# Kernel tuning notes

Measured on AMD Instinct MI355X. Metric: run time of the kernel, lower is better.

The kernel has to match this reference:

```python
import jax, jax.numpy as jnp
import numpy as np

N_EMB = 256
HEAD_SIZE = 64
B, S = 4, 4096


def setup_inputs() -> dict:
    key = jax.random.key(0)
    k1, k2, k3, k4 = jax.random.split(key, 4)
    return {
        "ini_emb": jax.random.normal(k1, (B, S, N_EMB), dtype=jnp.float32),
        "wk": jax.random.normal(k2, (N_EMB, HEAD_SIZE), dtype=jnp.float32) * (N_EMB ** -0.5),
        "wq": jax.random.normal(k3, (N_EMB, HEAD_SIZE), dtype=jnp.float32) * (N_EMB ** -0.5),
        "wv": jax.random.normal(k4, (N_EMB, HEAD_SIZE), dtype=jnp.float32) * (N_EMB ** -0.5),
    }


def reference(ini_emb, wk, wq, wv):
    # projections: [B,S,E] @ [E,H] -> [B,S,H]
    k = ini_emb @ wk
    q = ini_emb @ wq
    v = ini_emb @ wv
    # scores: [B,S,S]; NOTE: source scales by n_emb**-0.5, not head_size**-0.5
    scores = jnp.einsum("bqh,bkh->bqk", q, k) * (N_EMB ** -0.5)
    attn = jax.nn.softmax(scores, axis=-1)
    # output: [B,S,H]
    return jnp.einsum("bqk,bkh->bqh", attn, v)
```

## Files before the change

kernel.cpp:

```cpp
#include <hip/hip_runtime.h>


typedef short short4v __attribute__((ext_vector_type(4)));
typedef short short8v __attribute__((ext_vector_type(8)));
typedef float floatx4 __attribute__((ext_vector_type(4)));
typedef unsigned short u16;
typedef unsigned int u32;

#define SEQ 4096
#define EMB 256
#define HD 64
#define PADA 264

static __device__ __forceinline__ u16 f2bf(float x) {
    union { float f; unsigned u; } v; v.f = x;
    unsigned r = v.u + 0x7FFFu + ((v.u >> 16) & 1u);
    return (u16)(r >> 16);
}

static __device__ __forceinline__ short4v pack_bf4(float a, float b, float c, float d) {
    union { u32 u[2]; short4v s; } x;
    x.u[0] = (u32)f2bf(a) | ((u32)f2bf(b) << 16);
    x.u[1] = (u32)f2bf(c) | ((u32)f2bf(d) << 16);
    return x.s;
}

__global__ __launch_bounds__(256) void prep_w(
    const float* __restrict__ wk, const float* __restrict__ wq, const float* __restrict__ wv,
    u16* __restrict__ wt) {
    const int nt = blockIdx.x;
    const int t = threadIdx.x;
#pragma unroll
    for (int ss = 0; ss < 2; ++ss) {
        int slot = t + ss * 256;
        int kc = slot >> 6, lane = slot & 63;
        int ln15 = lane & 15, lq = lane >> 4;
        int cg = nt * 16 + ln15;
        int mat = cg >> 6, col = cg & 63;
        const float* W = (mat == 0) ? wq : (mat == 1) ? wk : wv;
        const float s = (mat == 0) ? 0.0625f * 1.44269504088896f : 1.0f;
        u32 w4[4];
#pragma unroll
        for (int p = 0; p < 2; ++p) {
#pragma unroll
            for (int d = 0; d < 2; ++d) {
                int e0 = kc * 32 + lq * 8 + p * 4 + d * 2;
                u16 lo = f2bf(W[(e0 + 0) * HD + col] * s);
                u16 hi = f2bf(W[(e0 + 1) * HD + col] * s);
                w4[p * 2 + d] = (u32)lo | ((u32)hi << 16);
            }
        }
        u32* dst = (u32*)wt + ((size_t)(nt * 8 + kc) * 64 + lane) * 4;
        *(uint4*)dst = make_uint4(w4[0], w4[1], w4[2], w4[3]);
    }
}

__global__ __launch_bounds__(256) void proj_mfma(
    const float* __restrict__ emb, const u16* __restrict__ wt,
    u16* __restrict__ qb, u16* __restrict__ kb, u16* __restrict__ vbt) {
    __shared__ u16 a_s[16 * PADA];
    const int t = threadIdx.x;
    const int lane = t & 63;
    const int wave = t >> 6;
    const int ln15 = lane & 15;
    const int lq = lane >> 4;
    const size_t row0 = (size_t)blockIdx.x * 16;

#pragma unroll
    for (int c = 0; c < 4; ++c) {
        int f = t + c * 256;
        int row = f >> 6, e4 = (f & 63) * 4;
        float4 v = *(const float4*)(emb + (row0 + row) * EMB + e4);
        ushort4 o;
        o.x = f2bf(v.x); o.y = f2bf(v.y); o.z = f2bf(v.z); o.w = f2bf(v.w);
        *(ushort4*)&a_s[row * PADA + e4] = o;
    }
    __syncthreads();

    floatx4 acc[3];
#pragma unroll
    for (int j = 0; j < 3; ++j) {
        floatx4 z = { 0.f, 0.f, 0.f, 0.f };
        acc[j] = z;
    }

#pragma unroll
    for (int kc = 0; kc < 8; ++kc) {
        short8v a = *(const short8v*)&a_s[ln15 * PADA + kc * 32 + lq * 8];
#pragma unroll
        for (int j = 0; j < 3; ++j) {
            short8v b = *(const short8v*)(wt + (((size_t)(wave * 3 + j) * 8 + kc) * 64 + lane) * 8);
            acc[j] = __builtin_amdgcn_mfma_f32_16x16x32_bf16(a, b, acc[j], 0, 0, 0);
        }
    }

#pragma unroll
    for (int j = 0; j < 3; ++j) {
        int cg = (wave * 3 + j) * 16 + ln15;
        int mat = cg >> 6, col = cg & 63;
        if (mat < 2) {
            u16* O = (mat == 0) ? qb : kb;
#pragma unroll
            for (int r = 0; r < 4; ++r)
                O[(row0 + lq * 4 + r) * HD + col] = f2bf(acc[j][r]);
        } else {
            ushort4 o4;
            o4.x = f2bf(acc[j][0]); o4.y = f2bf(acc[j][1]);
            o4.z = f2bf(acc[j][2]); o4.w = f2bf(acc[j][3]);
            size_t bidx = row0 >> 12;
            size_t sl = (row0 & 4095) + lq * 4;
            *(ushort4*)&vbt[(bidx * 64 + col) * SEQ + sl] = o4;
        }
    }
}

__global__ __launch_bounds__(256) void attn_kernel(
    const u16* __restrict__ qb, const u16* __restrict__ kb, const u16* __restrict__ vbt,
    float* __restrict__ po, float* __restrict__ pml) {
    __shared__ float ored[64 * 66];
    __shared__ float lred[4 * 64];

    const int t = threadIdx.x;
    const int lane = t & 63;
    const int wave = t >> 6;
    const int ln15 = lane & 15;
    const int lq = lane >> 4;

    const int part = blockIdx.x;
    const int b = part >> 8;
    const int qt = (part >> 2) & 63;
    const int split = part & 3;
    const int q0 = qt * 64;

    const u16* __restrict__ qpb = qb + ((size_t)b * SEQ + q0) * HD;
    const u16* __restrict__ kpb = kb + (size_t)b * SEQ * HD;
    const u16* __restrict__ vpb = vbt + (size_t)b * HD * SEQ;

    short8v qf[4][2];
#pragma unroll
    for (int nt = 0; nt < 4; ++nt)
#pragma unroll
        for (int h = 0; h < 2; ++h)
            qf[nt][h] = *(const short8v*)(qpb + (size_t)(nt * 16 + ln15) * HD + h * 32 + lq * 8);

    floatx4 oacc[4][4];
#pragma unroll
    for (int ht = 0; ht < 4; ++ht)
#pragma unroll
        for (int nt = 0; nt < 4; ++nt) {
            floatx4 z = { 0.f, 0.f, 0.f, 0.f };
            oacc[ht][nt] = z;
        }
    float lacc[4] = { 0.f, 0.f, 0.f, 0.f };

    for (int tt = 0; tt < 16; ++tt) {
        const int kw = (split * 16 + tt) * 64 + wave * 16;

        short8v kf0 = *(const short8v*)(kpb + (size_t)(kw + ln15) * HD + lq * 8);
        short8v kf1 = *(const short8v*)(kpb + (size_t)(kw + ln15) * HD + 32 + lq * 8);
        short4v vf[4];
#pragma unroll
        for (int ht = 0; ht < 4; ++ht)
            vf[ht] = *(const short4v*)(vpb + (size_t)(ht * 16 + ln15) * SEQ + kw + lq * 4);

        floatx4 s[4];
#pragma unroll
        for (int nt = 0; nt < 4; ++nt) {
            floatx4 z = { 0.f, 0.f, 0.f, 0.f };
            s[nt] = __builtin_amdgcn_mfma_f32_16x16x32_bf16(kf0, qf[nt][0], z, 0, 0, 0);
            s[nt] = __builtin_amdgcn_mfma_f32_16x16x32_bf16(kf1, qf[nt][1], s[nt], 0, 0, 0);
        }

        short4v pf[4];
#pragma unroll
        for (int nt = 0; nt < 4; ++nt) {
            float p0 = __builtin_amdgcn_exp2f(s[nt][0]);
            float p1 = __builtin_amdgcn_exp2f(s[nt][1]);
            float p2 = __builtin_amdgcn_exp2f(s[nt][2]);
            float p3 = __builtin_amdgcn_exp2f(s[nt][3]);
            lacc[nt] += (p0 + p1) + (p2 + p3);
            pf[nt] = pack_bf4(p0, p1, p2, p3);
        }

#pragma unroll
        for (int ht = 0; ht < 4; ++ht)
#pragma unroll
            for (int nt = 0; nt < 4; ++nt)
                oacc[ht][nt] = __builtin_amdgcn_mfma_f32_16x16x16bf16_1k(
                    vf[ht], pf[nt], oacc[ht][nt], 0, 0, 0);
    }

#pragma unroll
    for (int nt = 0; nt < 4; ++nt) {
        lacc[nt] += __shfl_xor(lacc[nt], 16);
        lacc[nt] += __shfl_xor(lacc[nt], 32);
    }
    if (lq == 0) {
#pragma unroll
        for (int nt = 0; nt < 4; ++nt)
            lred[wave * 64 + nt * 16 + ln15] = lacc[nt];
    }

    for (int s4 = 0; s4 < 4; ++s4) {
        if (wave == s4) {
#pragma unroll
            for (int ht = 0; ht < 4; ++ht)
#pragma unroll
                for (int nt = 0; nt < 4; ++nt)
#pragma unroll
                    for (int r = 0; r < 4; ++r) {
                        int idx = (ht * 16 + lq * 4 + r) * 66 + nt * 16 + ln15;
                        if (s4 == 0) ored[idx] = oacc[ht][nt][r];
                        else ored[idx] += oacc[ht][nt][r];
                    }
        }
        __syncthreads();
    }

    float* __restrict__ pob = po + (size_t)part * 4096;
#pragma unroll
    for (int i = 0; i < 16; ++i) {
        int f = t + i * 256;
        pob[f] = ored[(f >> 6) * 66 + (f & 63)];
    }
    if (t < 64)
        pml[part * 64 + t] = lred[t] + lred[64 + t] + lred[128 + t] + lred[192 + t];
}

__global__ __launch_bounds__(256) void reduce_kernel(
    const float* __restrict__ po, const float* __restrict__ pml,
    float* __restrict__ out) {
    __shared__ float os[64 * 67];
    __shared__ float ls[64];
    const int t = threadIdx.x;
    const int part0 = blockIdx.x * 4;
    const int bq = blockIdx.x;

#pragma unroll
    for (int i = 0; i < 16; ++i) {
        int f = t + i * 256;
        float a = po[(size_t)(part0 + 0) * 4096 + f] + po[(size_t)(part0 + 1) * 4096 + f]
                + po[(size_t)(part0 + 2) * 4096 + f] + po[(size_t)(part0 + 3) * 4096 + f];
        os[(f >> 6) * 67 + (f & 63)] = a;
    }
    if (t < 64)
        ls[t] = pml[(part0 + 0) * 64 + t] + pml[(part0 + 1) * 64 + t]
              + pml[(part0 + 2) * 64 + t] + pml[(part0 + 3) * 64 + t];
    __syncthreads();

    const size_t orow0 = ((size_t)(bq >> 6) * SEQ + (size_t)(bq & 63) * 64);
#pragma unroll
    for (int i = 0; i < 4; ++i) {
        int f4 = t + i * 256;
        int q = f4 >> 4, h4 = (f4 & 15) * 4;
        float inv = 1.0f / ls[q];
        float4 r;
        r.x = os[(h4 + 0) * 67 + q] * inv;
        r.y = os[(h4 + 1) * 67 + q] * inv;
        r.z = os[(h4 + 2) * 67 + q] * inv;
        r.w = os[(h4 + 3) * 67 + q] * inv;
        *(float4*)&out[(orow0 + q) * HD + h4] = r;
    }
}

extern "C" void kernel_launch(void* const* d_in, const int* in_sizes, int n_in,
                              void* d_out, int out_size, void* d_ws, size_t ws_size,
                              hipStream_t stream) {
    const float* emb = (const float*)d_in[0];
    const float* wk  = (const float*)d_in[1];
    const float* wq  = (const float*)d_in[2];
    const float* wv  = (const float*)d_in[3];

    u16* qb  = (u16*)d_ws;
    u16* kb  = (u16*)((char*)d_ws + (size_t)2 * 1024 * 1024);
    u16* vbt = (u16*)((char*)d_ws + (size_t)4 * 1024 * 1024);
    u16* wt  = (u16*)((char*)d_ws + (size_t)6 * 1024 * 1024);
    float* po  = (float*)((char*)d_ws + (size_t)6 * 1024 * 1024 + 256 * 1024);
    float* pml = (float*)((char*)d_ws + (size_t)22 * 1024 * 1024 + 256 * 1024);
    float* out = (float*)d_out;

    prep_w<<<12, 256, 0, stream>>>(wk, wq, wv, wt);
    proj_mfma<<<1024, 256, 0, stream>>>(emb, wt, qb, kb, vbt);
    attn_kernel<<<1024, 256, 0, stream>>>(qb, kb, vbt, po, pml);
    reduce_kernel<<<256, 256, 0, stream>>>(po, pml, out);
}
```

Baseline: 139.3 us.

## Prefetch K tiles, use hardware bf16 packing, vectorize partial output reduction

```diff
diff --git a/kernel.cpp b/kernel.cpp
--- a/kernel.cpp
+++ b/kernel.cpp
@@ -11,6 +11,7 @@
 #define EMB 256
 #define HD 64
 #define PADA 264
+#define OSTR 68
 
 static __device__ __forceinline__ u16 f2bf(float x) {
     union { float f; unsigned u; } v; v.f = x;
@@ -18,10 +19,16 @@
     return (u16)(r >> 16);
 }
 
+static __device__ __forceinline__ u32 cvt_pk_bf16(float a, float b) {
+    u32 r;
+    asm("v_cvt_pk_bf16_f32 %0, %1, %2" : "=v"(r) : "v"(a), "v"(b));
+    return r;
+}
+
 static __device__ __forceinline__ short4v pack_bf4(float a, float b, float c, float d) {
     union { u32 u[2]; short4v s; } x;
-    x.u[0] = (u32)f2bf(a) | ((u32)f2bf(b) << 16);
-    x.u[1] = (u32)f2bf(c) | ((u32)f2bf(d) << 16);
+    x.u[0] = cvt_pk_bf16(a, b);
+    x.u[1] = cvt_pk_bf16(c, d);
     return x.s;
 }
 
@@ -71,9 +78,9 @@
         int f = t + c * 256;
         int row = f >> 6, e4 = (f & 63) * 4;
         float4 v = *(const float4*)(emb + (row0 + row) * EMB + e4);
-        ushort4 o;
-        o.x = f2bf(v.x); o.y = f2bf(v.y); o.z = f2bf(v.z); o.w = f2bf(v.w);
-        *(ushort4*)&a_s[row * PADA + e4] = o;
+        u32 lo = cvt_pk_bf16(v.x, v.y);
+        u32 hi = cvt_pk_bf16(v.z, v.w);
+        *(uint2*)&a_s[row * PADA + e4] = make_uint2(lo, hi);
     }
     __syncthreads();
 
@@ -104,20 +111,71 @@
             for (int r = 0; r < 4; ++r)
                 O[(row0 + lq * 4 + r) * HD + col] = f2bf(acc[j][r]);
         } else {
-            ushort4 o4;
-            o4.x = f2bf(acc[j][0]); o4.y = f2bf(acc[j][1]);
-            o4.z = f2bf(acc[j][2]); o4.w = f2bf(acc[j][3]);
+            u32 lo = cvt_pk_bf16(acc[j][0], acc[j][1]);
+            u32 hi = cvt_pk_bf16(acc[j][2], acc[j][3]);
             size_t bidx = row0 >> 12;
             size_t sl = (row0 & 4095) + lq * 4;
-            *(ushort4*)&vbt[(bidx * 64 + col) * SEQ + sl] = o4;
-        }
-    }
+            *(uint2*)&vbt[(bidx * 64 + col) * SEQ + sl] = make_uint2(lo, hi);
+        }
+    }
+}
+
+
+template <bool PF>
+static __device__ __forceinline__ void attn_step(
+    const int tt, const int split, const int wave, const int ln15, const int lq,
+    const u16* __restrict__ kpb, const u16* __restrict__ vpb,
+    const short8v (&qf)[4][2], const short8v k0c, const short8v k1c,
+    short8v& k0n, short8v& k1n,
+    floatx4 (&oacc)[4][4], float (&lacc)[4]) {
+    const int kw = (split * 16 + tt) * 64 + wave * 16;
+
+    short4v vf[4];
+#pragma unroll
+    for (int ht = 0; ht < 4; ++ht)
+        vf[ht] = *(const short4v*)(vpb + (size_t)(ht * 16 + ln15) * SEQ + kw + lq * 4);
+
+    if (PF) {
+        const int kwn = kw + 64;
+        k0n = *(const short8v*)(kpb + (size_t)(kwn + ln15) * HD + lq * 8);
+        k1n = *(const short8v*)(kpb + (size_t)(kwn + ln15) * HD + 32 + lq * 8);
+    }
+
+    floatx4 s[4];
+    __builtin_amdgcn_s_setprio(1);
+#pragma unroll
+    for (int nt = 0; nt < 4; ++nt) {
+        floatx4 z = { 0.f, 0.f, 0.f, 0.f };
+        s[nt] = __builtin_amdgcn_mfma_f32_16x16x32_bf16(k0c, qf[nt][0], z, 0, 0, 0);
+        s[nt] = __builtin_amdgcn_mfma_f32_16x16x32_bf16(k1c, qf[nt][1], s[nt], 0, 0, 0);
+    }
+    __builtin_amdgcn_s_setprio(0);
+
+    short4v pf[4];
+#pragma unroll
+    for (int nt = 0; nt < 4; ++nt) {
+        float p0 = __builtin_amdgcn_exp2f(s[nt][0]);
+        float p1 = __builtin_amdgcn_exp2f(s[nt][1]);
+        float p2 = __builtin_amdgcn_exp2f(s[nt][2]);
+        float p3 = __builtin_amdgcn_exp2f(s[nt][3]);
+        lacc[nt] += (p0 + p1) + (p2 + p3);
+        pf[nt] = pack_bf4(p0, p1, p2, p3);
+    }
+
+    __builtin_amdgcn_s_setprio(1);
+#pragma unroll
+    for (int ht = 0; ht < 4; ++ht)
+#pragma unroll
+        for (int nt = 0; nt < 4; ++nt)
+            oacc[ht][nt] = __builtin_amdgcn_mfma_f32_16x16x16bf16_1k(
+                vf[ht], pf[nt], oacc[ht][nt], 0, 0, 0);
+    __builtin_amdgcn_s_setprio(0);
 }
 
 __global__ __launch_bounds__(256) void attn_kernel(
     const u16* __restrict__ qb, const u16* __restrict__ kb, const u16* __restrict__ vbt,
     float* __restrict__ po, float* __restrict__ pml) {
-    __shared__ float ored[64 * 66];
+    __shared__ float ored[64 * OSTR];
     __shared__ float lred[4 * 64];
 
     const int t = threadIdx.x;
@@ -153,41 +211,19 @@
         }
     float lacc[4] = { 0.f, 0.f, 0.f, 0.f };
 
-    for (int tt = 0; tt < 16; ++tt) {
-        const int kw = (split * 16 + tt) * 64 + wave * 16;
-
-        short8v kf0 = *(const short8v*)(kpb + (size_t)(kw + ln15) * HD + lq * 8);
-        short8v kf1 = *(const short8v*)(kpb + (size_t)(kw + ln15) * HD + 32 + lq * 8);
-        short4v vf[4];
-#pragma unroll
-        for (int ht = 0; ht < 4; ++ht)
-            vf[ht] = *(const short4v*)(vpb + (size_t)(ht * 16 + ln15) * SEQ + kw + lq * 4);
-
-        floatx4 s[4];
-#pragma unroll
-        for (int nt = 0; nt < 4; ++nt) {
-            floatx4 z = { 0.f, 0.f, 0.f, 0.f };
-            s[nt] = __builtin_amdgcn_mfma_f32_16x16x32_bf16(kf0, qf[nt][0], z, 0, 0, 0);
-            s[nt] = __builtin_amdgcn_mfma_f32_16x16x32_bf16(kf1, qf[nt][1], s[nt], 0, 0, 0);
-        }
-
-        short4v pf[4];
-#pragma unroll
-        for (int nt = 0; nt < 4; ++nt) {
-            float p0 = __builtin_amdgcn_exp2f(s[nt][0]);
-            float p1 = __builtin_amdgcn_exp2f(s[nt][1]);
-            float p2 = __builtin_amdgcn_exp2f(s[nt][2]);
-            float p3 = __builtin_amdgcn_exp2f(s[nt][3]);
-            lacc[nt] += (p0 + p1) + (p2 + p3);
-            pf[nt] = pack_bf4(p0, p1, p2, p3);
-        }
-
-#pragma unroll
-        for (int ht = 0; ht < 4; ++ht)
-#pragma unroll
-            for (int nt = 0; nt < 4; ++nt)
-                oacc[ht][nt] = __builtin_amdgcn_mfma_f32_16x16x16bf16_1k(
-                    vf[ht], pf[nt], oacc[ht][nt], 0, 0, 0);
+    short8v kA0, kA1, kB0, kB1;
+    {
+        const int kw0 = (split * 16) * 64 + wave * 16;
+        kA0 = *(const short8v*)(kpb + (size_t)(kw0 + ln15) * HD + lq * 8);
+        kA1 = *(const short8v*)(kpb + (size_t)(kw0 + ln15) * HD + 32 + lq * 8);
+    }
+
+#pragma unroll 1
+    for (int tth = 0; tth < 8; ++tth) {
+        attn_step<true>(2 * tth,     split, wave, ln15, lq, kpb, vpb, qf,
+                        kA0, kA1, kB0, kB1, oacc, lacc);
+        attn_step<true>(2 * tth + 1, split, wave, ln15, lq, kpb, vpb, qf,
+                        kB0, kB1, kA0, kA1, oacc, lacc);
     }
 
 #pragma unroll
@@ -204,24 +240,28 @@
     for (int s4 = 0; s4 < 4; ++s4) {
         if (wave == s4) {
 #pragma unroll
-            for (int ht = 0; ht < 4; ++ht)
-#pragma unroll
-                for (int nt = 0; nt < 4; ++nt)
-#pragma unroll
-                    for (int r = 0; r < 4; ++r) {
-                        int idx = (ht * 16 + lq * 4 + r) * 66 + nt * 16 + ln15;
-                        if (s4 == 0) ored[idx] = oacc[ht][nt][r];
-                        else ored[idx] += oacc[ht][nt][r];
+            for (int nt = 0; nt < 4; ++nt)
+#pragma unroll
+                for (int ht = 0; ht < 4; ++ht) {
+                    int idx = (nt * 16 + ln15) * OSTR + ht * 16 + lq * 4;
+                    if (s4 == 0) {
+                        *(floatx4*)&ored[idx] = oacc[ht][nt];
+                    } else {
+                        floatx4 old = *(floatx4*)&ored[idx];
+                        old += oacc[ht][nt];
+                        *(floatx4*)&ored[idx] = old;
                     }
+                }
         }
         __syncthreads();
     }
 
     float* __restrict__ pob = po + (size_t)part * 4096;
 #pragma unroll
-    for (int i = 0; i < 16; ++i) {
-        int f = t + i * 256;
-        pob[f] = ored[(f >> 6) * 66 + (f & 63)];
+    for (int i = 0; i < 4; ++i) {
+        int f4 = t + i * 256;
+        int q = f4 >> 4, h4 = (f4 & 15) * 4;
+        *(float4*)&pob[q * HD + h4] = *(float4*)&ored[q * OSTR + h4];
     }
     if (t < 64)
         pml[part * 64 + t] = lred[t] + lred[64 + t] + lred[128 + t] + lred[192 + t];
@@ -230,36 +270,38 @@
 __global__ __launch_bounds__(256) void reduce_kernel(
     const float* __restrict__ po, const float* __restrict__ pml,
     float* __restrict__ out) {
-    __shared__ float os[64 * 67];
     __shared__ float ls[64];
     const int t = threadIdx.x;
     const int part0 = blockIdx.x * 4;
     const int bq = blockIdx.x;
 
-#pragma unroll
-    for (int i = 0; i < 16; ++i) {
-        int f = t + i * 256;
-        float a = po[(size_t)(part0 + 0) * 4096 + f] + po[(size_t)(part0 + 1) * 4096 + f]
-                + po[(size_t)(part0 + 2) * 4096 + f] + po[(size_t)(part0 + 3) * 4096 + f];
-        os[(f >> 6) * 67 + (f & 63)] = a;
-    }
     if (t < 64)
         ls[t] = pml[(part0 + 0) * 64 + t] + pml[(part0 + 1) * 64 + t]
               + pml[(part0 + 2) * 64 + t] + pml[(part0 + 3) * 64 + t];
     __syncthreads();
 
-    const size_t orow0 = ((size_t)(bq >> 6) * SEQ + (size_t)(bq & 63) * 64);
+    const float* __restrict__ p0 = po + (size_t)(part0 + 0) * 4096;
+    const float* __restrict__ p1 = po + (size_t)(part0 + 1) * 4096;
+    const float* __restrict__ p2 = po + (size_t)(part0 + 2) * 4096;
+    const float* __restrict__ p3 = po + (size_t)(part0 + 3) * 4096;
+    float* __restrict__ ob = out + (((size_t)(bq >> 6) * SEQ + (size_t)(bq & 63) * 64)) * HD;
+
 #pragma unroll
     for (int i = 0; i < 4; ++i) {
         int f4 = t + i * 256;
-        int q = f4 >> 4, h4 = (f4 & 15) * 4;
+        int f = f4 * 4;
+        int q = f4 >> 4;
+        float4 a = *(const float4*)&p0[f];
+        float4 c = *(const float4*)&p1[f];
+        float4 d = *(const float4*)&p2[f];
+        float4 e = *(const float4*)&p3[f];
         float inv = 1.0f / ls[q];
         float4 r;
-        r.x = os[(h4 + 0) * 67 + q] * inv;
-        r.y = os[(h4 + 1) * 67 + q] * inv;
-        r.z = os[(h4 + 2) * 67 + q] * inv;
-        r.w = os[(h4 + 3) * 67 + q] * inv;
-        *(float4*)&out[(orow0 + q) * HD + h4] = r;
+        r.x = (a.x + c.x + d.x + e.x) * inv;
+        r.y = (a.y + c.y + d.y + e.y) * inv;
+        r.z = (a.z + c.z + d.z + e.z) * inv;
+        r.w = (a.w + c.w + d.w + e.w) * inv;
+        *(float4*)&ob[f] = r;
     }
 }
 
```

Result: faster. 136.4 us (-2.1%).
